# Optimization experiments

Measured on AMD Instinct MI355X. Metric: run time of the kernel, lower is better.

## Reference

```python
import jax, jax.numpy as jnp
import numpy as np

B, C, T, H = 64, 800, 512, 1024
IN = 2 * C  # 1600, matches hardcoded input_size in PCLSTMCell


def setup_inputs() -> dict:
    key = jax.random.key(0)
    ks = jax.random.split(key, 24)
    s = 0.02
    d = {}
    d["x"] = jax.random.normal(ks[0], (B, C, T), jnp.float32)
    d["y"] = jax.random.normal(ks[1], (B, C, T), jnp.float32)
    d["subject_id"] = jax.random.normal(ks[2], (B, 87), jnp.float32)
    for n_i, n in enumerate(["f", "i", "u", "o"]):
        d[f"W_{n}x"] = jax.random.normal(ks[3 + 4 * n_i], (IN, H), jnp.float32) * s
        d[f"b_{n}x"] = jnp.zeros((H,), jnp.float32)
        d[f"W_{n}h"] = jax.random.normal(ks[4 + 4 * n_i], (H, H), jnp.float32) * s
        d[f"b_{n}h"] = jnp.zeros((H,), jnp.float32)
    d["W_init"] = jax.random.normal(ks[20], (87, H), jnp.float32) * s
    d["b_init"] = jnp.zeros((H,), jnp.float32)
    return d


def reference(x, y, subject_id,
              W_fx, b_fx, W_fh, b_fh,
              W_ix, b_ix, W_ih, b_ih,
              W_ux, b_ux, W_uh, b_uh,
              W_ox, b_ox, W_oh, b_oh,
              W_init, b_init):
    Bc, Cc, Tc = x.shape
    Hc = W_fh.shape[0]
    # y_prev[t] = y[t-1], zeros at t=0 (matches torch.zeros at t==0)
    y_prev = jnp.concatenate([jnp.zeros_like(y[..., :1]), y[..., :-1]], axis=-1)
    # torch.stack((x_i, y_prev), dim=-1).view(B,-1): channel-interleaved [x0,y0,x1,y1,...]
    xs = jnp.stack([x, y_prev], axis=2)                    # [B, C, 2, T]
    xs = jnp.moveaxis(xs, -1, 0).reshape(Tc, Bc, 2 * Cc)    # [T, B, 2C]
    # fuse the 4 input-side gate GEMMs and precompute over all timesteps
    Wx = jnp.concatenate([W_fx, W_ix, W_ux, W_ox], axis=1)  # [2C, 4H]
    bx = jnp.concatenate([b_fx, b_ix, b_ux, b_ox])          # [4H]
    gx = jnp.einsum('tbi,ig->tbg', xs, Wx) + bx             # [T, B, 4H]
    Wh = jnp.concatenate([W_fh, W_ih, W_uh, W_oh], axis=1)  # [H, 4H]
    bh = jnp.concatenate([b_fh, b_ih, b_uh, b_oh])

    h0 = jnp.zeros((Bc, Hc), x.dtype)
    c0 = subject_id @ W_init + b_init                       # initilaizer(subject_id)

    def step(carry, gx_t):
        h, c = carry
        g = gx_t + h @ Wh + bh
        f, i, u, o = jnp.split(g, 4, axis=-1)
        f = jax.nn.sigmoid(f)
        i = jax.nn.sigmoid(i)
        u = jnp.tanh(u)
        o = jax.nn.sigmoid(o)
        c = c * f + i * u
        h = o * jnp.tanh(c)
        return (h, c), h

    (_, c_fin), hs = jax.lax.scan(step, (h0, c0), gx)       # hs: [T, B, H]
    h_seq = jnp.moveaxis(hs, 0, -1)                          # [B, H, T]
    return h_seq, c_fin
```

## Files before the change

### kernel.cpp

```cpp
#include <hip/hip_runtime.h>

typedef __attribute__((ext_vector_type(8))) short short8;
typedef __attribute__((ext_vector_type(4))) float f32x4;
typedef __attribute__((ext_vector_type(4))) _Float16 f16x4;
typedef __attribute__((ext_vector_type(4))) unsigned int u32x4;
typedef unsigned long long u64_t;

#define DI __device__ __forceinline__

DI unsigned short f2bf(float f) {
  unsigned int u = __float_as_uint(f);
  u += 0x7FFFu + ((u >> 16) & 1u);
  return (unsigned short)(u >> 16);
}

DI void gload_lds16(const void* g, void* l) {
  __builtin_amdgcn_global_load_lds(
      (const __attribute__((address_space(1))) unsigned int*)g,
      (__attribute__((address_space(3))) unsigned int*)l, 16, 0, 0);
}

DI float sigm(float x) { return 1.f / (1.f + __expf(-x)); }
DI float tanh_(float x) { return 1.f - 2.f / (__expf(2.f * x) + 1.f); }

DI u32x4 h_load16(const void* p) {
  u32x4 r;
  asm volatile("global_load_dwordx4 %0, %1, off sc0 sc1" : "=v"(r) : "v"(p) : "memory");
  return r;
}

static constexpr size_t OFF_WXT  = 0;
static constexpr size_t OFF_WHT  = 13107200;
static constexpr size_t OFF_BSUM = OFF_WHT + 8388608;
static constexpr size_t OFF_XS   = OFF_BSUM + 16384;
static constexpr size_t OFF_GX   = OFF_XS + 104857600;
static constexpr size_t OFF_HBUF = OFF_GX + 268435456;
static constexpr size_t OFF_BAR  = OFF_HBUF + 262144;
static constexpr size_t WS_NEED  = OFF_BAR + 32768;

__global__ __launch_bounds__(256) void pack_w(
    const float* __restrict__ s0, const float* __restrict__ s1,
    const float* __restrict__ s2, const float* __restrict__ s3,
    unsigned short* __restrict__ dst, int K) {
  __shared__ float tile[32][33];
  const int tx = threadIdx.x & 31, ty = threadIdx.x >> 5;
  const int kt = blockIdx.x, nt = blockIdx.y;
  const int q = (nt * 32) >> 10;
  const float* src = (q == 0) ? s0 : (q == 1) ? s1 : (q == 2) ? s2 : s3;
  const int cbase = (nt * 32) & 1023;
#pragma unroll
  for (int i = 0; i < 4; ++i) {
    int k = kt * 32 + ty + i * 8;
    tile[ty + i * 8][tx] = src[(size_t)k * 1024 + cbase + tx];
  }
  __syncthreads();
#pragma unroll
  for (int i = 0; i < 4; ++i) {
    int n = nt * 32 + ty + i * 8;
    dst[(size_t)n * K + kt * 32 + tx] = f2bf(tile[tx][ty + i * 8]);
  }
}

__global__ __launch_bounds__(256) void pack_bias(
    const float* bx0, const float* bx1, const float* bx2, const float* bx3,
    const float* bh0, const float* bh1, const float* bh2, const float* bh3,
    float* __restrict__ bsum) {
  int n = blockIdx.x * 256 + threadIdx.x;
  int q = n >> 10, j = n & 1023;
  const float* bx = (q == 0) ? bx0 : (q == 1) ? bx1 : (q == 2) ? bx2 : bx3;
  const float* bh = (q == 0) ? bh0 : (q == 1) ? bh1 : (q == 2) ? bh2 : bh3;
  bsum[n] = bx[j] + bh[j];
}

__global__ __launch_bounds__(256) void xs_pack(
    const float* __restrict__ x, const float* __restrict__ y,
    unsigned int* __restrict__ xs32) {
  __shared__ float xt[32][33], yt[32][33];
  const int tx = threadIdx.x & 31, ty = threadIdx.x >> 5;
  const int tt = blockIdx.x, ct = blockIdx.y, b = blockIdx.z;
#pragma unroll
  for (int i = 0; i < 4; ++i) {
    int c = ct * 32 + ty + i * 8;
    int t = tt * 32 + tx;
    size_t base = ((size_t)b * 800 + c) * 512;
    xt[ty + i * 8][tx] = x[base + t];
    yt[ty + i * 8][tx] = (t == 0) ? 0.f : y[base + t - 1];
  }
  __syncthreads();
#pragma unroll
  for (int i = 0; i < 4; ++i) {
    int t = tt * 32 + ty + i * 8;
    int c = ct * 32 + tx;
    unsigned int pk = ((unsigned int)f2bf(yt[tx][ty + i * 8]) << 16) |
                      (unsigned int)f2bf(xt[tx][ty + i * 8]);
    xs32[((size_t)t * 64 + b) * 800 + c] = pk;
  }
}

__global__ __launch_bounds__(512, 2) void gemm_gx(
    const unsigned short* __restrict__ xs, const unsigned short* __restrict__ Wxt,
    const float* __restrict__ bsum, _Float16* __restrict__ gx) {
  __shared__ __align__(16) char smem[98304];
  const int tid = threadIdx.x;
  const int w = tid >> 6, l = tid & 63;
  const int l15 = l & 15, l4 = l >> 4;
  const int wm = w >> 2, wn = w & 3;
  const int u = (blockIdx.x & 7) * 256 + (blockIdx.x >> 3);
  const int bm = u >> 4, bn = u & 15;

  const unsigned short* abase0 = xs + (size_t)(bm * 256) * 1600;
  const unsigned short* bbase0 = Wxt + (size_t)(bn * 256) * 1600;

  const int c0 = w * 64 + l;
  const int r0 = c0 >> 2, k0 = c0 & 3;
  const int c1 = 512 + c0;
  const int r1 = c1 >> 2, k1 = c1 & 3;
  const int dst0 = w * 1024;
  const int dst1 = 8192 + w * 1024;

#define STAGE(kt2, slot)                                                        \
  {                                                                             \
    const unsigned short* ab = abase0 + (kt2) * 32;                             \
    const unsigned short* bb = bbase0 + (kt2) * 32;                             \
    char* Asl = smem + (slot) * 16384;                                          \
    char* Bsl = smem + 49152 + (slot) * 16384;                                  \
    gload_lds16(ab + (size_t)r0 * 1600 + k0 * 8, Asl + dst0);                   \
    gload_lds16(bb + (size_t)r0 * 1600 + k0 * 8, Bsl + dst0);                   \
    gload_lds16(ab + (size_t)r1 * 1600 + k1 * 8, Asl + dst1);                   \
    gload_lds16(bb + (size_t)r1 * 1600 + k1 * 8, Bsl + dst1);                   \
  }

  f32x4 acc[8][4];
#pragma unroll
  for (int i = 0; i < 8; ++i)
#pragma unroll
    for (int j = 0; j < 4; ++j) acc[i][j] = (f32x4){0.f, 0.f, 0.f, 0.f};

  STAGE(0, 0);
  STAGE(1, 1);
  STAGE(2, 2);

  int slot = 0;
  for (int t = 0; t < 50; ++t) {
    if (t < 48) {
      asm volatile("s_waitcnt vmcnt(8)" ::: "memory");
    } else {
      asm volatile("s_waitcnt vmcnt(0)" ::: "memory");
    }
    __builtin_amdgcn_s_barrier();
    const char* Asl = smem + slot * 16384;
    const char* Bsl = smem + 49152 + slot * 16384;
    short8 af[8], bf[4];
#pragma unroll
    for (int mf = 0; mf < 8; ++mf)
      af[mf] = *(const short8*)(Asl + (wm * 128 + mf * 16 + l15) * 64 + l4 * 16);
#pragma unroll
    for (int nf = 0; nf < 4; ++nf)
      bf[nf] = *(const short8*)(Bsl + (wn * 64 + nf * 16 + l15) * 64 + l4 * 16);
    __builtin_amdgcn_s_setprio(1);
#pragma unroll
    for (int mf = 0; mf < 8; ++mf)
#pragma unroll
      for (int nf = 0; nf < 4; ++nf)
        acc[mf][nf] = __builtin_amdgcn_mfma_f32_16x16x32_bf16(
            af[mf], bf[nf], acc[mf][nf], 0, 0, 0);
    __builtin_amdgcn_s_setprio(0);
    __builtin_amdgcn_s_barrier();
    asm volatile("" ::: "memory");
    if (t + 3 < 50) STAGE(t + 3, slot);
    slot = (slot == 2) ? 0 : slot + 1;
  }
#undef STAGE

#pragma unroll
  for (int nf = 0; nf < 4; ++nf) {
    int col = bn * 256 + wn * 64 + nf * 16 + l15;
    float bs = bsum[col];
    int colp = (col & 1023) * 4 + (col >> 10);
#pragma unroll
    for (int mf = 0; mf < 8; ++mf) {
      int row0 = bm * 256 + wm * 128 + mf * 16 + l4 * 4;
#pragma unroll
      for (int j = 0; j < 4; ++j)
        gx[(size_t)(row0 + j) * 4096 + colp] = (_Float16)(acc[mf][nf][j] + bs);
    }
  }
}

__global__ __launch_bounds__(512, 2) void lstm_seq(
    const _Float16* __restrict__ gx, const unsigned short* __restrict__ Wht,
    const float* __restrict__ subj, const float* __restrict__ Winit,
    const float* __restrict__ binit, float* __restrict__ out,
    unsigned int* __restrict__ hbuf, unsigned int* __restrict__ bar) {
  const int gg  = blockIdx.x & 7;
  const int cwg = blockIdx.x >> 3;
  const int tid = threadIdx.x;
  const int w = tid >> 6, l = tid & 63;
  const int l15 = l & 15, l4 = l >> 4;
  const int ws = w & 1, kq = w >> 1;
  const int ghc = cwg * 32 + ws * 16 + l15;

  __shared__ __align__(16) char smem[98304];

  short8 Bf[32];
  {
    const unsigned short* wp =
        Wht + (size_t)(cwg * 32 + ws * 16 + l15) * 1024 + kq * 256 + l4 * 8;
#pragma unroll
    for (int g = 0; g < 4; ++g)
#pragma unroll
      for (int ks = 0; ks < 8; ++ks)
        Bf[g * 8 + ks] = *(const short8*)(wp + (size_t)g * 1048576 + ks * 32);
  }

  float c[4], hq[4][8];
  if (w < 2 && l4 < 2) {
#pragma unroll
    for (int j = 0; j < 4; ++j) {
      int b = gg * 8 + l4 * 4 + j;
      float a = binit[ghc];
      for (int k = 0; k < 87; ++k) a += subj[b * 87 + k] * Winit[k * 1024 + ghc];
      c[j] = a;
    }
  }

  unsigned int* flags = bar + gg * 1024;

  const int so0 = tid * 16;
  const int so1 = (tid + 512) * 16;
  const int sw0 = so0 ^ (((so0 >> 11) & 7) << 4);
  const int sw1 = so1 ^ (((so1 >> 11) & 7) << 4);

  for (int t8 = 0; t8 < 64; ++t8) {
#pragma unroll
    for (int s = 0; s < 8; ++s) {
      const int t = t8 * 8 + s;
      const int cur = s & 1, nxt = cur ^ 1;
      if (w == 7) {
        const unsigned tgt = (unsigned)t;
        for (;;) {
          unsigned f = 0xFFFFFFFFu;
          if (l < 32)
            f = __hip_atomic_load(flags + l * 32, __ATOMIC_RELAXED,
                                  __HIP_MEMORY_SCOPE_AGENT);
          if (__all(f >= tgt)) break;
          __builtin_amdgcn_s_sleep(1);
        }
      }
      __syncthreads();
      {
        const char* src = (const char*)hbuf + (size_t)(gg * 2 + cur) * 16384;
        u32x4 v0 = h_load16(src + so0);
        u32x4 v1 = h_load16(src + so1);
        asm volatile("s_waitcnt vmcnt(0)" ::: "memory");
        *(u32x4*)(smem + sw0) = v0;
        *(u32x4*)(smem + sw1) = v1;
      }
      f16x4 gxq[4];
      if (w < 2 && l4 < 2) {
        const _Float16* gp =
            gx + ((size_t)(t * 64 + gg * 8 + l4 * 4)) * 4096 + ghc * 4;
#pragma unroll
        for (int j = 0; j < 4; ++j) gxq[j] = *(const f16x4*)(gp + (size_t)j * 4096);
      }
      __syncthreads();
      f32x4 acc[4];
#pragma unroll
      for (int g = 0; g < 4; ++g) acc[g] = (f32x4){0.f, 0.f, 0.f, 0.f};
#pragma unroll
      for (int ks = 0; ks < 8; ++ks) {
        short8 a = *(const short8*)(
            smem + (((l15 & 7) * 2048 + kq * 512 + ks * 64 + l4 * 16) ^ ((l15 & 7) << 4)));
#pragma unroll
        for (int g = 0; g < 4; ++g)
          acc[g] = __builtin_amdgcn_mfma_f32_16x16x32_bf16(a, Bf[g * 8 + ks], acc[g], 0, 0, 0);
      }
      if (w >= 2) {
        char* pb = smem + 16384 + (size_t)(ws * 3 + kq - 1) * 4096;
#pragma unroll
        for (int g = 0; g < 4; ++g) *(f32x4*)(pb + g * 1024 + l * 16) = acc[g];
      }
      __syncthreads();
      if (w < 2) {
        f32x4 red[4];
#pragma unroll
        for (int g = 0; g < 4; ++g) {
          red[g] = acc[g];
#pragma unroll
          for (int kk = 0; kk < 3; ++kk)
            red[g] += *(const f32x4*)(smem + 16384 + (size_t)(ws * 3 + kk) * 4096 +
                                      g * 1024 + l * 16);
        }
        if (l4 < 2) {
#pragma unroll
          for (int j = 0; j < 4; ++j) {
            float fv = sigm(red[0][j] + (float)gxq[j][0]);
            float iv = sigm(red[1][j] + (float)gxq[j][1]);
            float uv = tanh_(red[2][j] + (float)gxq[j][2]);
            float ov = sigm(red[3][j] + (float)gxq[j][3]);
            c[j] = c[j] * fv + iv * uv;
            float hv = ov * tanh_(c[j]);
            hq[j][s] = hv;
            float hn = __shfl_xor(hv, 1);
            if (!(l15 & 1)) {
              unsigned int pk = (unsigned int)f2bf(hv) | ((unsigned int)f2bf(hn) << 16);
              __hip_atomic_store(
                  hbuf + (gg * 2 + nxt) * 4096 + (l4 * 4 + j) * 512 +
                      cwg * 16 + ws * 8 + (l15 >> 1),
                  pk, __ATOMIC_RELAXED, __HIP_MEMORY_SCOPE_AGENT);
            }
          }
        }
      }
      asm volatile("s_waitcnt vmcnt(0)" ::: "memory");
      __syncthreads();
      if (tid == 0)
        __hip_atomic_store(flags + cwg * 32, (unsigned)(t + 1),
                           __ATOMIC_RELAXED, __HIP_MEMORY_SCOPE_AGENT);
    }
    if (w < 2 && l4 < 2) {
      int tb = t8 * 8;
#pragma unroll
      for (int j = 0; j < 4; ++j) {
        f32x4 v0 = {hq[j][0], hq[j][1], hq[j][2], hq[j][3]};
        f32x4 v1 = {hq[j][4], hq[j][5], hq[j][6], hq[j][7]};
        float* op = out + (size_t)(gg * 8 + l4 * 4 + j) * 524288 + (size_t)ghc * 512 + tb;
        *(f32x4*)op = v0;
        *(f32x4*)(op + 4) = v1;
      }
    }
  }
  if (w < 2 && l4 < 2) {
#pragma unroll
    for (int j = 0; j < 4; ++j)
      out[33554432 + (size_t)(gg * 8 + l4 * 4 + j) * 1024 + ghc] = c[j];
  }
}

extern "C" void kernel_launch(void* const* d_in, const int* in_sizes, int n_in,
                              void* d_out, int out_size, void* d_ws, size_t ws_size,
                              hipStream_t stream) {
  (void)in_sizes; (void)n_in; (void)out_size;
  if (ws_size < WS_NEED) return;

  const float* x     = (const float*)d_in[0];
  const float* y     = (const float*)d_in[1];
  const float* subj  = (const float*)d_in[2];
  const float* W_fx  = (const float*)d_in[3];
  const float* b_fx  = (const float*)d_in[4];
  const float* W_fh  = (const float*)d_in[5];
  const float* b_fh  = (const float*)d_in[6];
  const float* W_ix  = (const float*)d_in[7];
  const float* b_ix  = (const float*)d_in[8];
  const float* W_ih  = (const float*)d_in[9];
  const float* b_ih  = (const float*)d_in[10];
  const float* W_ux  = (const float*)d_in[11];
  const float* b_ux  = (const float*)d_in[12];
  const float* W_uh  = (const float*)d_in[13];
  const float* b_uh  = (const float*)d_in[14];
  const float* W_ox  = (const float*)d_in[15];
  const float* b_ox  = (const float*)d_in[16];
  const float* W_oh  = (const float*)d_in[17];
  const float* b_oh  = (const float*)d_in[18];
  const float* Winit = (const float*)d_in[19];
  const float* binit = (const float*)d_in[20];
  float* out = (float*)d_out;

  char* ws = (char*)d_ws;
  unsigned short* Wxt  = (unsigned short*)(ws + OFF_WXT);
  unsigned short* Wht  = (unsigned short*)(ws + OFF_WHT);
  float*          bsum = (float*)(ws + OFF_BSUM);
  unsigned int*   xs32 = (unsigned int*)(ws + OFF_XS);
  _Float16*       gx   = (_Float16*)(ws + OFF_GX);
  unsigned int*   hbuf = (unsigned int*)(ws + OFF_HBUF);
  unsigned int*   bar  = (unsigned int*)(ws + OFF_BAR);

  hipMemsetAsync(ws + OFF_HBUF, 0, WS_NEED - OFF_HBUF, stream);

  pack_w<<<dim3(50, 128), 256, 0, stream>>>(W_fx, W_ix, W_ux, W_ox, Wxt, 1600);
  pack_w<<<dim3(32, 128), 256, 0, stream>>>(W_fh, W_ih, W_uh, W_oh, Wht, 1024);
  pack_bias<<<16, 256, 0, stream>>>(b_fx, b_ix, b_ux, b_ox, b_fh, b_ih, b_uh, b_oh, bsum);
  xs_pack<<<dim3(16, 25, 64), 256, 0, stream>>>(x, y, xs32);
  gemm_gx<<<2048, 512, 0, stream>>>((const unsigned short*)xs32, Wxt, bsum, gx);

  const _Float16* gxc = gx;
  const unsigned short* whtc = Wht;
  void* ka[8] = {(void*)&gxc, (void*)&whtc, (void*)&subj, (void*)&Winit,
                 (void*)&binit, (void*)&out, (void*)&hbuf, (void*)&bar};
  hipError_t e = hipLaunchCooperativeKernel((const void*)lstm_seq, dim3(256), dim3(512),
                                            ka, 0, stream);
  if (e != hipSuccess) {
    lstm_seq<<<256, 512, 0, stream>>>(gxc, whtc, subj, Winit, binit, out, hbuf, bar);
  }
}
```

Before: 2.712 ms.

## Interleave gate columns and give each wave full-K recurrent MFMA without LDS reduction

Packs the input and recurrent weights with gate-interleaved column order (hidden*4+gate), so each wave in the sequential LSTM kernel owns 16 permuted columns (4 hidden units x 4 gates) and runs the full K=1024 reduction itself. This removes the split-K partial-sum write to LDS, the second __syncthreads and the cross-wave reduction on every timestep. Gate values are gathered across lanes with shuffles and all 8 waves now do the pointwise work. The cost is a longer serial MFMA chain per wave, eased by two accumulators, plus extra shuffles, and only a quarter of lanes store outputs.

Measured after the change: 3.013 ms. 11.1% more time.

```diff
diff --git a/kernel.cpp b/kernel.cpp
--- a/kernel.cpp
+++ b/kernel.cpp
@@ -41,7 +41,7 @@
 __global__ __launch_bounds__(256) void pack_w(
     const float* __restrict__ s0, const float* __restrict__ s1,
     const float* __restrict__ s2, const float* __restrict__ s3,
-    unsigned short* __restrict__ dst, int K) {
+    unsigned short* __restrict__ dst, int K, int perm) {
   __shared__ float tile[32][33];
   const int tx = threadIdx.x & 31, ty = threadIdx.x >> 5;
   const int kt = blockIdx.x, nt = blockIdx.y;
@@ -57,7 +57,8 @@
 #pragma unroll
   for (int i = 0; i < 4; ++i) {
     int n = nt * 32 + ty + i * 8;
-    dst[(size_t)n * K + kt * 32 + tx] = f2bf(tile[tx][ty + i * 8]);
+    int np = perm ? ((n & 1023) * 4 + (n >> 10)) : n;
+    dst[(size_t)np * K + kt * 32 + tx] = f2bf(tile[tx][ty + i * 8]);
   }
 }
 
@@ -98,7 +99,7 @@
 }
 
 __global__ __launch_bounds__(512, 2) void gemm_gx(
-    const unsigned short* __restrict__ xs, const unsigned short* __restrict__ Wxt,
+    const unsigned short* __restrict__ xs, const unsigned short* __restrict__ Wxtp,
     const float* __restrict__ bsum, _Float16* __restrict__ gx) {
   __shared__ __align__(16) char smem[98304];
   const int tid = threadIdx.x;
@@ -109,7 +110,7 @@
   const int bm = u >> 4, bn = u & 15;
 
   const unsigned short* abase0 = xs + (size_t)(bm * 256) * 1600;
-  const unsigned short* bbase0 = Wxt + (size_t)(bn * 256) * 1600;
+  const unsigned short* bbase0 = Wxtp + (size_t)(bn * 256) * 1600;
 
   const int c0 = w * 64 + l;
   const int r0 = c0 >> 2, k0 = c0 & 3;
@@ -174,9 +175,8 @@
 
 #pragma unroll
   for (int nf = 0; nf < 4; ++nf) {
-    int col = bn * 256 + wn * 64 + nf * 16 + l15;
-    float bs = bsum[col];
-    int colp = (col & 1023) * 4 + (col >> 10);
+    int colp = bn * 256 + wn * 64 + nf * 16 + l15;
+    float bs = bsum[(colp & 3) * 1024 + (colp >> 2)];
 #pragma unroll
     for (int mf = 0; mf < 8; ++mf) {
       int row0 = bm * 256 + wm * 128 + mf * 16 + l4 * 4;
@@ -188,7 +188,7 @@
 }
 
 __global__ __launch_bounds__(512, 2) void lstm_seq(
-    const _Float16* __restrict__ gx, const unsigned short* __restrict__ Wht,
+    const _Float16* __restrict__ gx, const unsigned short* __restrict__ Whtp,
     const float* __restrict__ subj, const float* __restrict__ Winit,
     const float* __restrict__ binit, float* __restrict__ out,
     unsigned int* __restrict__ hbuf, unsigned int* __restrict__ bar) {
@@ -197,24 +197,20 @@
   const int tid = threadIdx.x;
   const int w = tid >> 6, l = tid & 63;
   const int l15 = l & 15, l4 = l >> 4;
-  const int ws = w & 1, kq = w >> 1;
-  const int ghc = cwg * 32 + ws * 16 + l15;
+  const int ghc = cwg * 32 + w * 4 + (l15 >> 2);
+  const int colp = cwg * 128 + w * 16 + l15;
 
   __shared__ __align__(16) char smem[98304];
 
   short8 Bf[32];
   {
-    const unsigned short* wp =
-        Wht + (size_t)(cwg * 32 + ws * 16 + l15) * 1024 + kq * 256 + l4 * 8;
-#pragma unroll
-    for (int g = 0; g < 4; ++g)
-#pragma unroll
-      for (int ks = 0; ks < 8; ++ks)
-        Bf[g * 8 + ks] = *(const short8*)(wp + (size_t)g * 1048576 + ks * 32);
+    const unsigned short* wp = Whtp + (size_t)colp * 1024 + l4 * 8;
+#pragma unroll
+    for (int kk = 0; kk < 32; ++kk) Bf[kk] = *(const short8*)(wp + kk * 32);
   }
 
   float c[4], hq[4][8];
-  if (w < 2 && l4 < 2) {
+  if (l4 < 2) {
 #pragma unroll
     for (int j = 0; j < 4; ++j) {
       int b = gg * 8 + l4 * 4 + j;
@@ -256,59 +252,43 @@
         *(u32x4*)(smem + sw0) = v0;
         *(u32x4*)(smem + sw1) = v1;
       }
-      f16x4 gxq[4];
-      if (w < 2 && l4 < 2) {
-        const _Float16* gp =
-            gx + ((size_t)(t * 64 + gg * 8 + l4 * 4)) * 4096 + ghc * 4;
-#pragma unroll
-        for (int j = 0; j < 4; ++j) gxq[j] = *(const f16x4*)(gp + (size_t)j * 4096);
+      float gxv[4];
+      if (l4 < 2) {
+        const _Float16* gp = gx + ((size_t)(t * 64 + gg * 8 + l4 * 4)) * 4096 + colp;
+#pragma unroll
+        for (int j = 0; j < 4; ++j) gxv[j] = (float)gp[(size_t)j * 4096];
       }
       __syncthreads();
-      f32x4 acc[4];
-#pragma unroll
-      for (int g = 0; g < 4; ++g) acc[g] = (f32x4){0.f, 0.f, 0.f, 0.f};
-#pragma unroll
-      for (int ks = 0; ks < 8; ++ks) {
-        short8 a = *(const short8*)(
-            smem + (((l15 & 7) * 2048 + kq * 512 + ks * 64 + l4 * 16) ^ ((l15 & 7) << 4)));
-#pragma unroll
-        for (int g = 0; g < 4; ++g)
-          acc[g] = __builtin_amdgcn_mfma_f32_16x16x32_bf16(a, Bf[g * 8 + ks], acc[g], 0, 0, 0);
-      }
-      if (w >= 2) {
-        char* pb = smem + 16384 + (size_t)(ws * 3 + kq - 1) * 4096;
-#pragma unroll
-        for (int g = 0; g < 4; ++g) *(f32x4*)(pb + g * 1024 + l * 16) = acc[g];
-      }
-      __syncthreads();
-      if (w < 2) {
-        f32x4 red[4];
-#pragma unroll
-        for (int g = 0; g < 4; ++g) {
-          red[g] = acc[g];
-#pragma unroll
-          for (int kk = 0; kk < 3; ++kk)
-            red[g] += *(const f32x4*)(smem + 16384 + (size_t)(ws * 3 + kk) * 4096 +
-                                      g * 1024 + l * 16);
-        }
-        if (l4 < 2) {
-#pragma unroll
-          for (int j = 0; j < 4; ++j) {
-            float fv = sigm(red[0][j] + (float)gxq[j][0]);
-            float iv = sigm(red[1][j] + (float)gxq[j][1]);
-            float uv = tanh_(red[2][j] + (float)gxq[j][2]);
-            float ov = sigm(red[3][j] + (float)gxq[j][3]);
-            c[j] = c[j] * fv + iv * uv;
-            float hv = ov * tanh_(c[j]);
-            hq[j][s] = hv;
-            float hn = __shfl_xor(hv, 1);
-            if (!(l15 & 1)) {
-              unsigned int pk = (unsigned int)f2bf(hv) | ((unsigned int)f2bf(hn) << 16);
-              __hip_atomic_store(
-                  hbuf + (gg * 2 + nxt) * 4096 + (l4 * 4 + j) * 512 +
-                      cwg * 16 + ws * 8 + (l15 >> 1),
-                  pk, __ATOMIC_RELAXED, __HIP_MEMORY_SCOPE_AGENT);
-            }
+      f32x4 a0 = {0.f, 0.f, 0.f, 0.f}, a1 = {0.f, 0.f, 0.f, 0.f};
+#pragma unroll
+      for (int kk = 0; kk < 32; kk += 2) {
+        short8 v0 = *(const short8*)(
+            smem + (((l15 & 7) * 2048 + kk * 64 + l4 * 16) ^ ((l15 & 7) << 4)));
+        a0 = __builtin_amdgcn_mfma_f32_16x16x32_bf16(v0, Bf[kk], a0, 0, 0, 0);
+        short8 v1 = *(const short8*)(
+            smem + (((l15 & 7) * 2048 + (kk + 1) * 64 + l4 * 16) ^ ((l15 & 7) << 4)));
+        a1 = __builtin_amdgcn_mfma_f32_16x16x32_bf16(v1, Bf[kk + 1], a1, 0, 0, 0);
+      }
+      f32x4 acc = a0 + a1;
+      if (l4 < 2) {
+#pragma unroll
+        for (int j = 0; j < 4; ++j) {
+          float g = acc[j] + gxv[j];
+          int base = l & ~3;
+          float fv = sigm(__shfl(g, base));
+          float iv = sigm(__shfl(g, base + 1));
+          float uv = tanh_(__shfl(g, base + 2));
+          float ov = sigm(__shfl(g, base + 3));
+          c[j] = c[j] * fv + iv * uv;
+          float hv = ov * tanh_(c[j]);
+          hq[j][s] = hv;
+          float hn = __shfl(hv, l ^ 4);
+          if ((l15 & 7) == 0) {
+            unsigned int pk = (unsigned int)f2bf(hv) | ((unsigned int)f2bf(hn) << 16);
+            __hip_atomic_store(
+                hbuf + (gg * 2 + nxt) * 4096 + (l4 * 4 + j) * 512 +
+                    cwg * 16 + w * 2 + (l15 >> 3),
+                pk, __ATOMIC_RELAXED, __HIP_MEMORY_SCOPE_AGENT);
           }
         }
       }
@@ -318,7 +298,7 @@
         __hip_atomic_store(flags + cwg * 32, (unsigned)(t + 1),
                            __ATOMIC_RELAXED, __HIP_MEMORY_SCOPE_AGENT);
     }
-    if (w < 2 && l4 < 2) {
+    if (l4 < 2 && (l15 & 3) == 0) {
       int tb = t8 * 8;
 #pragma unroll
       for (int j = 0; j < 4; ++j) {
@@ -330,7 +310,7 @@
       }
     }
   }
-  if (w < 2 && l4 < 2) {
+  if (l4 < 2 && (l15 & 3) == 0) {
 #pragma unroll
     for (int j = 0; j < 4; ++j)
       out[33554432 + (size_t)(gg * 8 + l4 * 4 + j) * 1024 + ghc] = c[j];
@@ -377,8 +357,8 @@
 
   hipMemsetAsync(ws + OFF_HBUF, 0, WS_NEED - OFF_HBUF, stream);
 
-  pack_w<<<dim3(50, 128), 256, 0, stream>>>(W_fx, W_ix, W_ux, W_ox, Wxt, 1600);
-  pack_w<<<dim3(32, 128), 256, 0, stream>>>(W_fh, W_ih, W_uh, W_oh, Wht, 1024);
+  pack_w<<<dim3(50, 128), 256, 0, stream>>>(W_fx, W_ix, W_ux, W_ox, Wxt, 1600, 1);
+  pack_w<<<dim3(32, 128), 256, 0, stream>>>(W_fh, W_ih, W_uh, W_oh, Wht, 1024, 1);
   pack_bias<<<16, 256, 0, stream>>>(b_fx, b_ix, b_ux, b_ox, b_fh, b_ih, b_uh, b_oh, bsum);
   xs_pack<<<dim3(16, 25, 64), 256, 0, stream>>>(x, y, xs32);
   gemm_gx<<<2048, 512, 0, stream>>>((const unsigned short*)xs32, Wxt, bsum, gx);
```
